# Optimization experiments

Hardware: AMD Instinct MI355X
Metric: run time of the kernel (lower is better)

## Reference

```python
import jax, jax.numpy as jnp
import numpy as np

N, E, F_IN, H, G, A, OUT = 50000, 800000, 128, 256, 64, 8, 1


def _lin(k, fi, fo):
    s = 1.0 / np.sqrt(fi)
    kw, kb = jax.random.split(k)
    W = jax.random.uniform(kw, (fi, fo), jnp.float32, -s, s)
    b = jax.random.uniform(kb, (fo,), jnp.float32, -s, s)
    return W, b


def setup_inputs() -> dict:
    key = jax.random.key(0)
    ks = jax.random.split(key, 12)
    x = jax.random.normal(ks[0], (N, F_IN), jnp.float32)
    edge_index = jax.random.randint(ks[1], (2, E), 0, N, dtype=jnp.int64)
    batch = jnp.sort(jax.random.randint(ks[2], (N,), 0, G, dtype=jnp.int64))
    graph_attr = jax.random.normal(ks[3], (G, A), jnp.float32)
    W1, b1 = _lin(ks[4], F_IN, H)
    W2, b2 = _lin(ks[5], H, H)
    W3, b3 = _lin(ks[6], H, H)
    fcW1, fcb1 = _lin(ks[7], H + A, H)
    fcW2, fcb2 = _lin(ks[8], H, OUT)
    ones = jnp.ones((H,), jnp.float32)
    zeros = jnp.zeros((H,), jnp.float32)
    return dict(x=x, graph_attr=graph_attr, edge_index=edge_index, batch=batch,
                W1=W1, b1=b1, W2=W2, b2=b2, W3=W3, b3=b3,
                g1=ones, be1=zeros, g2=ones, be2=zeros, g3=ones, be3=zeros,
                fcW1=fcW1, fcb1=fcb1, fcW2=fcW2, fcb2=fcb2)


def gcn_conv(x, W, b, src, dst, n):
    # PyG GCNConv: add self-loops, symmetric normalization, xW then scatter-add
    xw = x @ W  # [N, H]
    loop = jnp.arange(n)
    src2 = jnp.concatenate([src, loop])
    dst2 = jnp.concatenate([dst, loop])
    deg = jnp.zeros((n,), xw.dtype).at[dst2].add(1.0)
    dinv = jnp.where(deg > 0, jax.lax.rsqrt(deg), 0.0)
    norm = dinv[src2] * dinv[dst2]  # [E+N]
    out = jnp.zeros((n, xw.shape[1]), xw.dtype).at[dst2].add(xw[src2] * norm[:, None])
    return out + b


def layer_norm(x, g, b, eps=1e-5):
    m = x.mean(-1, keepdims=True)
    v = ((x - m) ** 2).mean(-1, keepdims=True)
    return (x - m) * jax.lax.rsqrt(v + eps) * g + b


def reference(x, graph_attr, edge_index, batch,
              W1, b1, W2, b2, W3, b3,
              g1, be1, g2, be2, g3, be3,
              fcW1, fcb1, fcW2, fcb2):
    src, dst = edge_index[0], edge_index[1]
    h = jax.nn.relu(layer_norm(gcn_conv(x, W1, b1, src, dst, N), g1, be1))
    h = jax.nn.relu(layer_norm(gcn_conv(h, W2, b2, src, dst, N), g2, be2))
    h = jax.nn.relu(layer_norm(gcn_conv(h, W3, b3, src, dst, N), g3, be3))
    # global mean pool over graph ids
    sums = jax.ops.segment_sum(h, batch, num_segments=G)
    cnts = jax.ops.segment_sum(jnp.ones((N,), h.dtype), batch, num_segments=G)
    pooled = sums / jnp.maximum(cnts, 1.0)[:, None]  # [G, H]
    z = jnp.concatenate([pooled, graph_attr.reshape(-1, A)], axis=1)
    z = jax.nn.relu(z @ fcW1 + fcb1)
    return z @ fcW2 + fcb2  # [G, OUT]
```

## Files before the change

### kernel.cpp

```cpp
#include <hip/hip_runtime.h>
#include <hip/hip_bf16.h>

#define N_NODES 50000
#define N_EDGES 800000
#define F_IN    128
#define H_DIM   256
#define G_NUM   64
#define A_DIM   8

#define NBUCKET 196
#define NCHUNK  391
#define CHUNK   2048
#define K4CAP   6144

typedef __attribute__((ext_vector_type(8))) short short8v;
typedef __attribute__((ext_vector_type(4))) float float4v;
typedef __attribute__((ext_vector_type(2))) float float2v;

__device__ __forceinline__ float b2f(unsigned short u) {
    return __uint_as_float(((unsigned int)u) << 16);
}
__device__ __forceinline__ unsigned short f2b(float v) {
    return __hip_bfloat16_raw(__float2bfloat16(v)).x;
}
__device__ __forceinline__ unsigned char f2fp8(float v) {
    return (unsigned char)(__builtin_amdgcn_cvt_pk_fp8_f32(v, v, 0, false) & 0xff);
}
__device__ __forceinline__ unsigned int pack2(float a, float b) {
    return (unsigned int)f2b(a) | ((unsigned int)f2b(b) << 16);
}
__device__ __forceinline__ void accadd16(float2v* a, uint4 v) {
    a[0] += __builtin_amdgcn_cvt_pk_f32_fp8((int)v.x, false);
    a[1] += __builtin_amdgcn_cvt_pk_f32_fp8((int)v.x, true);
    a[2] += __builtin_amdgcn_cvt_pk_f32_fp8((int)v.y, false);
    a[3] += __builtin_amdgcn_cvt_pk_f32_fp8((int)v.y, true);
    a[4] += __builtin_amdgcn_cvt_pk_f32_fp8((int)v.z, false);
    a[5] += __builtin_amdgcn_cvt_pk_f32_fp8((int)v.z, true);
    a[6] += __builtin_amdgcn_cvt_pk_f32_fp8((int)v.w, false);
    a[7] += __builtin_amdgcn_cvt_pk_f32_fp8((int)v.w, true);
}
__device__ __forceinline__ void accfma16(float2v* a, uint4 v, float w) {
    float2v w2 = {w, w};
    a[0] = __builtin_amdgcn_cvt_pk_f32_fp8((int)v.x, false) * w2 + a[0];
    a[1] = __builtin_amdgcn_cvt_pk_f32_fp8((int)v.x, true)  * w2 + a[1];
    a[2] = __builtin_amdgcn_cvt_pk_f32_fp8((int)v.y, false) * w2 + a[2];
    a[3] = __builtin_amdgcn_cvt_pk_f32_fp8((int)v.y, true)  * w2 + a[3];
    a[4] = __builtin_amdgcn_cvt_pk_f32_fp8((int)v.z, false) * w2 + a[4];
    a[5] = __builtin_amdgcn_cvt_pk_f32_fp8((int)v.z, true)  * w2 + a[5];
    a[6] = __builtin_amdgcn_cvt_pk_f32_fp8((int)v.w, false) * w2 + a[6];
    a[7] = __builtin_amdgcn_cvt_pk_f32_fp8((int)v.w, true)  * w2 + a[7];
}

#define SK 40


__global__ __launch_bounds__(512) void fuse0_kernel(const int* __restrict__ dst,
                                                    unsigned int* __restrict__ Hg,
                                                    const float* __restrict__ x,
                                                    const float* __restrict__ W1,
                                                    unsigned char* __restrict__ P8,
                                                    const float* __restrict__ W2,
                                                    unsigned short* __restrict__ Wt2,
                                                    const float* __restrict__ W3,
                                                    unsigned short* __restrict__ Wt3) {
    const int CB = NCHUNK;
    const int GB = (N_NODES + 127) / 128;
    int b = blockIdx.x, t = threadIdx.x;
    if (b < CB) {
        __shared__ unsigned int h[256];
        if (t < 256) h[t] = 0u;
        __syncthreads();
        int base = b * CHUNK;
        #pragma unroll
        for (int k = 0; k < 4; k++) {
            int i = base + k * 512 + t;
            if (i < N_EDGES) atomicAdd(&h[dst[i] >> 8], 1u);
        }
        __syncthreads();
        if (t < 256) Hg[(size_t)t * NCHUNK + b] = h[t];
        return;
    }
    b -= CB;
    if (b < GB) {
        __shared__ unsigned short As[128][SK];
        __shared__ unsigned short Bs[256][SK];
        int wave = t >> 6, lane = t & 63;
        int wm0 = (wave & 1) * 64, wn0 = (wave >> 1) * 64;
        int bm = b * 128;
        int l15 = lane & 15, lq = lane >> 4;
        float4v acc[4][4];
        #pragma unroll
        for (int i = 0; i < 4; i++)
            #pragma unroll
            for (int j = 0; j < 4; j++)
                acc[i][j] = (float4v){0.f, 0.f, 0.f, 0.f};

        for (int k0 = 0; k0 < F_IN; k0 += 32) {
            {
                int row = t >> 2, koff = (t & 3) * 8;
                short8v tmp = (short8v){0,0,0,0,0,0,0,0};
                if (bm + row < N_NODES) {
                    const float* xp = x + (size_t)(bm + row) * F_IN + k0 + koff;
                    float4 a0 = *(const float4*)xp;
                    float4 a1 = *(const float4*)(xp + 4);
                    tmp[0] = (short)f2b(a0.x); tmp[1] = (short)f2b(a0.y);
                    tmp[2] = (short)f2b(a0.z); tmp[3] = (short)f2b(a0.w);
                    tmp[4] = (short)f2b(a1.x); tmp[5] = (short)f2b(a1.y);
                    tmp[6] = (short)f2b(a1.z); tmp[7] = (short)f2b(a1.w);
                }
                *(short8v*)&As[row][koff] = tmp;
            }
            #pragma unroll
            for (int h = 0; h < 2; h++) {
                int c = t + h * 512;
                int n = c >> 2, koff = (c & 3) * 8;
                short8v tmp;
                #pragma unroll
                for (int kk = 0; kk < 8; kk++)
                    tmp[kk] = (short)f2b(W1[(size_t)(k0 + koff + kk) * H_DIM + n]);
                *(short8v*)&Bs[n][koff] = tmp;
            }
            __syncthreads();
            short8v af[4], bf[4];
            #pragma unroll
            for (int i = 0; i < 4; i++) {
                af[i] = *(const short8v*)&As[wm0 + i * 16 + l15][lq * 8];
                bf[i] = *(const short8v*)&Bs[wn0 + i * 16 + l15][lq * 8];
            }
            #pragma unroll
            for (int i = 0; i < 4; i++)
                #pragma unroll
                for (int j = 0; j < 4; j++)
                    acc[i][j] = __builtin_amdgcn_mfma_f32_16x16x32_bf16(af[i], bf[j], acc[i][j], 0, 0, 0);
            __syncthreads();
        }
        #pragma unroll
        for (int i = 0; i < 4; i++) {
            #pragma unroll
            for (int r = 0; r < 4; r++) {
                int row = bm + wm0 + i * 16 + lq * 4 + r;
                if (row < N_NODES) {
                    #pragma unroll
                    for (int j = 0; j < 4; j++) {
                        int col = wn0 + j * 16 + l15;
                        P8[(size_t)row * H_DIM + col] = f2fp8(acc[i][j][r]);
                    }
                }
            }
        }
        return;
    }
    b -= GB;
    int i = b * 512 + t;
    if (i < H_DIM * H_DIM) {
        int k = i >> 8, n = i & 255;
        Wt2[(size_t)n * H_DIM + k] = f2b(W2[i]);
    } else if (i < 2 * H_DIM * H_DIM) {
        int j = i - H_DIM * H_DIM;
        int k = j >> 8, n = j & 255;
        Wt3[(size_t)n * H_DIM + k] = f2b(W3[j]);
    }
}


__global__ __launch_bounds__(256) void scanH_kernel(unsigned int* __restrict__ Hg,
                                                    unsigned int* __restrict__ Btot) {
    __shared__ unsigned int tile[256];
    int b = blockIdx.x, t = threadIdx.x;
    unsigned int* row = Hg + (size_t)b * NCHUNK;
    int i0 = 2 * t, i1 = 2 * t + 1;
    unsigned int v0 = (i0 < NCHUNK) ? row[i0] : 0u;
    unsigned int v1 = (i1 < NCHUNK) ? row[i1] : 0u;
    unsigned int pair = v0 + v1;
    tile[t] = pair;
    __syncthreads();
    #pragma unroll
    for (int o = 1; o < 256; o <<= 1) {
        unsigned int add = (t >= o) ? tile[t - o] : 0u;
        __syncthreads();
        tile[t] += add;
        __syncthreads();
    }
    unsigned int excl = tile[t] - pair;
    if (i0 < NCHUNK) row[i0] = excl;
    if (i1 < NCHUNK) row[i1] = excl + v0;
    if (t == 255) Btot[b] = tile[255];
}

__global__ __launch_bounds__(256) void base_kernel(const unsigned int* __restrict__ Btot,
                                                   unsigned int* __restrict__ bucketBase,
                                                   const int* __restrict__ batch,
                                                   int* __restrict__ gstart,
                                                   int* __restrict__ rowptr,
                                                   float* __restrict__ pooled) {
    __shared__ unsigned int tile[256];
    int t = threadIdx.x;
    unsigned int v = (t < NBUCKET) ? Btot[t] : 0u;
    tile[t] = v;
    __syncthreads();
    #pragma unroll
    for (int o = 1; o < 256; o <<= 1) {
        unsigned int add = (t >= o) ? tile[t - o] : 0u;
        __syncthreads();
        tile[t] += add;
        __syncthreads();
    }
    if (t < NBUCKET) bucketBase[t] = tile[t] - v;
    if (t == NBUCKET - 1) bucketBase[NBUCKET] = tile[t];
    if (t == 0) rowptr[N_NODES] = N_EDGES;
    if (t <= G_NUM) {
        int lo = 0, hi = N_NODES;
        while (lo < hi) {
            int mid = (lo + hi) >> 1;
            if (batch[mid] < t) lo = mid + 1; else hi = mid;
        }
        gstart[t] = lo;
    }
    for (int i = t; i < G_NUM * H_DIM; i += 256) pooled[i] = 0.f;
}

__global__ __launch_bounds__(512) void scatter_kernel(const int* __restrict__ src,
                                                      const int* __restrict__ dst,
                                                      const unsigned int* __restrict__ Hg,
                                                      const unsigned int* __restrict__ bucketBase,
                                                      unsigned int* __restrict__ tmp) {
    __shared__ unsigned int off[256];
    int blk = blockIdx.x, t = threadIdx.x;
    if (t < 256)
        off[t] = (t < NBUCKET) ? (bucketBase[t] + Hg[(size_t)t * NCHUNK + blk]) : 0u;
    __syncthreads();
    int base = blk * CHUNK;
    #pragma unroll
    for (int k = 0; k < 4; k++) {
        int i = base + k * 512 + t;
        if (i < N_EDGES) {
            int d = dst[i], s = src[i];
            unsigned int slot = atomicAdd(&off[d >> 8], 1u);
            tmp[slot] = ((unsigned int)(d & 255) << 16) | (unsigned int)s;
        }
    }
}

__global__ __launch_bounds__(256) void finalize_kernel(const unsigned int* __restrict__ tmp,
                                                       const unsigned int* __restrict__ bucketBase,
                                                       int* __restrict__ rowptr,
                                                       float* __restrict__ dinv,
                                                       unsigned short* __restrict__ csr_src) {
    __shared__ unsigned int te[K4CAP];
    __shared__ unsigned int h2[256];
    __shared__ unsigned int sc[256];
    __shared__ unsigned int off2[256];
    int b = blockIdx.x, t = threadIdx.x;
    unsigned int beg = bucketBase[b], end = bucketBase[b + 1];
    int cnt = (int)(end - beg);
    bool lds_ok = (cnt <= K4CAP);
    h2[t] = 0u;
    __syncthreads();
    for (int i = t; i < cnt; i += 256) {
        unsigned int u = tmp[beg + i];
        if (lds_ok) te[i] = u;
        atomicAdd(&h2[u >> 16], 1u);
    }
    __syncthreads();
    unsigned int c = h2[t];
    sc[t] = c;
    __syncthreads();
    #pragma unroll
    for (int o = 1; o < 256; o <<= 1) {
        unsigned int add = (t >= o) ? sc[t - o] : 0u;
        __syncthreads();
        sc[t] += add;
        __syncthreads();
    }
    unsigned int excl = sc[t] - c;
    int v = (b << 8) + t;
    if (v < N_NODES) {
        rowptr[v] = (int)(beg + excl);
        dinv[v] = rsqrtf((float)c + 1.0f);
    }
    off2[t] = excl;
    __syncthreads();
    for (int i = t; i < cnt; i += 256) {
        unsigned int u = lds_ok ? te[i] : tmp[beg + i];
        unsigned int lo = u >> 16;
        unsigned int s2 = atomicAdd(&off2[lo], 1u);
        csr_src[beg + s2] = (unsigned short)(u & 0xFFFFu);
    }
}


__global__ __launch_bounds__(512) void gemm_f8(const unsigned short* __restrict__ A,
                                               const unsigned short* __restrict__ Bt,
                                               unsigned char* __restrict__ C8,
                                               const float* __restrict__ dinv,
                                               int M, int K) {
    __shared__ unsigned short As[128][SK];
    __shared__ unsigned short Bs[256][SK];
    int t = threadIdx.x;
    int wave = t >> 6, lane = t & 63;
    int wm0 = (wave & 1) * 64, wn0 = (wave >> 1) * 64;
    int bm = blockIdx.x * 128;
    int l15 = lane & 15, lq = lane >> 4;
    float4v acc[4][4];
    #pragma unroll
    for (int i = 0; i < 4; i++)
        #pragma unroll
        for (int j = 0; j < 4; j++)
            acc[i][j] = (float4v){0.f, 0.f, 0.f, 0.f};

    for (int k0 = 0; k0 < K; k0 += 32) {
        {
            int row = t >> 2, koff = (t & 3) * 8;
            uint4 va = make_uint4(0u, 0u, 0u, 0u);
            if (bm + row < M)
                va = *(const uint4*)(A + (size_t)(bm + row) * K + k0 + koff);
            *(uint4*)&As[row][koff] = va;
        }
        #pragma unroll
        for (int h = 0; h < 2; h++) {
            int c = t + h * 512;
            int row = c >> 2, koff = (c & 3) * 8;
            uint4 vb = *(const uint4*)(Bt + (size_t)row * K + k0 + koff);
            *(uint4*)&Bs[row][koff] = vb;
        }
        __syncthreads();
        short8v af[4], bf[4];
        #pragma unroll
        for (int i = 0; i < 4; i++) {
            af[i] = *(const short8v*)&As[wm0 + i * 16 + l15][lq * 8];
            bf[i] = *(const short8v*)&Bs[wn0 + i * 16 + l15][lq * 8];
        }
        #pragma unroll
        for (int i = 0; i < 4; i++)
            #pragma unroll
            for (int j = 0; j < 4; j++)
                acc[i][j] = __builtin_amdgcn_mfma_f32_16x16x32_bf16(af[i], bf[j], acc[i][j], 0, 0, 0);
        __syncthreads();
    }
    #pragma unroll
    for (int i = 0; i < 4; i++) {
        #pragma unroll
        for (int r = 0; r < 4; r++) {
            int row = bm + wm0 + i * 16 + lq * 4 + r;
            if (row < M) {
                float dv = dinv[row];
                #pragma unroll
                for (int j = 0; j < 4; j++) {
                    int col = wn0 + j * 16 + l15;
                    C8[(size_t)row * H_DIM + col] = f2fp8(dv * acc[i][j][r]);
                }
            }
        }
    }
}


template<bool W8, bool POOL>
__global__ __launch_bounds__(256) void gather_ns(const unsigned char* __restrict__ xw,
                                                 unsigned short* __restrict__ out,
                                                 const int* __restrict__ rowptr,
                                                 const unsigned short* __restrict__ csr_src,
                                                 const float* __restrict__ dinv,
                                                 const float* __restrict__ bias,
                                                 const float* __restrict__ gamma,
                                                 const float* __restrict__ beta,
                                                 const int* __restrict__ batch,
                                                 float* __restrict__ pooled) {
    __shared__ float sh[POOL ? 16 * 260 : 4];
    __shared__ int gid_s[POOL ? 16 : 4];
    int lane = threadIdx.x & 63;
    int wave = threadIdx.x >> 6;
    int p = lane & 15;
    int gbase = lane & 48;
    int nl = wave * 4 + (lane >> 4);
    int node = blockIdx.x * 16 + nl;
    int beg = rowptr[node];
    int deg = rowptr[node + 1] - beg;
    float d = dinv[node];
    const unsigned char* xp = xw + (size_t)p * 16;

    float2v acc2[8];
    #pragma unroll
    for (int k = 0; k < 8; k++) acc2[k] = (float2v){0.f, 0.f};

    {
        uint4 v = *(const uint4*)(xp + (size_t)node * H_DIM);
        if constexpr (W8) accfma16(acc2, v, d);
        else              accadd16(acc2, v);
    }

    int sv = 0; float wv = 0.f;
    if (p < deg) {
        sv = (int)csr_src[beg + p];
        if constexpr (W8) wv = dinv[sv];
    }

    for (int b0 = 0; b0 < deg; b0 += 16) {
        int m = deg - b0; if (m > 16) m = 16;
        int sv_n = 0; float wv_n = 0.f;
        int rem = deg - b0 - 16;
        if (rem > 0 && p < rem) {
            sv_n = (int)csr_src[beg + b0 + 16 + p];
            if constexpr (W8) wv_n = dinv[sv_n];
        }
        int j = 0;
        for (; j + 8 <= m; j += 8) {
            int s0 = __shfl(sv, gbase | j, 64);
            int s1 = __shfl(sv, gbase | (j + 1), 64);
            int s2 = __shfl(sv, gbase | (j + 2), 64);
            int s3 = __shfl(sv, gbase | (j + 3), 64);
            int s4 = __shfl(sv, gbase | (j + 4), 64);
            int s5 = __shfl(sv, gbase | (j + 5), 64);
            int s6 = __shfl(sv, gbase | (j + 6), 64);
            int s7 = __shfl(sv, gbase | (j + 7), 64);
            uint4 v0 = *(const uint4*)(xp + (size_t)s0 * H_DIM);
            uint4 v1 = *(const uint4*)(xp + (size_t)s1 * H_DIM);
            uint4 v2 = *(const uint4*)(xp + (size_t)s2 * H_DIM);
            uint4 v3 = *(const uint4*)(xp + (size_t)s3 * H_DIM);
            uint4 v4 = *(const uint4*)(xp + (size_t)s4 * H_DIM);
            uint4 v5 = *(const uint4*)(xp + (size_t)s5 * H_DIM);
            uint4 v6 = *(const uint4*)(xp + (size_t)s6 * H_DIM);
            uint4 v7 = *(const uint4*)(xp + (size_t)s7 * H_DIM);
            if constexpr (W8) {
                float w0 = __shfl(wv, gbase | j, 64);
                float w1 = __shfl(wv, gbase | (j + 1), 64);
                float w2 = __shfl(wv, gbase | (j + 2), 64);
                float w3 = __shfl(wv, gbase | (j + 3), 64);
                float w4 = __shfl(wv, gbase | (j + 4), 64);
                float w5 = __shfl(wv, gbase | (j + 5), 64);
                float w6 = __shfl(wv, gbase | (j + 6), 64);
                float w7 = __shfl(wv, gbase | (j + 7), 64);
                accfma16(acc2, v0, w0); accfma16(acc2, v1, w1);
                accfma16(acc2, v2, w2); accfma16(acc2, v3, w3);
                accfma16(acc2, v4, w4); accfma16(acc2, v5, w5);
                accfma16(acc2, v6, w6); accfma16(acc2, v7, w7);
            } else {
                accadd16(acc2, v0); accadd16(acc2, v1);
                accadd16(acc2, v2); accadd16(acc2, v3);
                accadd16(acc2, v4); accadd16(acc2, v5);
                accadd16(acc2, v6); accadd16(acc2, v7);
            }
        }
        for (; j + 4 <= m; j += 4) {
            int s0 = __shfl(sv, gbase | j, 64);
            int s1 = __shfl(sv, gbase | (j + 1), 64);
            int s2 = __shfl(sv, gbase | (j + 2), 64);
            int s3 = __shfl(sv, gbase | (j + 3), 64);
            uint4 v0 = *(const uint4*)(xp + (size_t)s0 * H_DIM);
            uint4 v1 = *(const uint4*)(xp + (size_t)s1 * H_DIM);
            uint4 v2 = *(const uint4*)(xp + (size_t)s2 * H_DIM);
            uint4 v3 = *(const uint4*)(xp + (size_t)s3 * H_DIM);
            if constexpr (W8) {
                float w0 = __shfl(wv, gbase | j, 64);
                float w1 = __shfl(wv, gbase | (j + 1), 64);
                float w2 = __shfl(wv, gbase | (j + 2), 64);
                float w3 = __shfl(wv, gbase | (j + 3), 64);
                accfma16(acc2, v0, w0); accfma16(acc2, v1, w1);
                accfma16(acc2, v2, w2); accfma16(acc2, v3, w3);
            } else {
                accadd16(acc2, v0); accadd16(acc2, v1);
                accadd16(acc2, v2); accadd16(acc2, v3);
            }
        }
        for (; j < m; ++j) {
            int s0 = __shfl(sv, gbase | j, 64);
            uint4 v0 = *(const uint4*)(xp + (size_t)s0 * H_DIM);
            if constexpr (W8) {
                float w0 = __shfl(wv, gbase | j, 64);
                accfma16(acc2, v0, w0);
            } else {
                accadd16(acc2, v0);
            }
        }
        sv = sv_n; wv = wv_n;
    }

    float v[16];
    #pragma unroll
    for (int k = 0; k < 8; k++) { v[2 * k] = d * acc2[k].x; v[2 * k + 1] = d * acc2[k].y; }

    #pragma unroll
    for (int q = 0; q < 4; q++) {
        float4 bi = ((const float4*)bias)[p * 4 + q];
        v[q * 4 + 0] += bi.x; v[q * 4 + 1] += bi.y;
        v[q * 4 + 2] += bi.z; v[q * 4 + 3] += bi.w;
    }
    float s = 0.f, ss = 0.f;
    #pragma unroll
    for (int k = 0; k < 16; k++) { s += v[k]; ss += v[k] * v[k]; }
    #pragma unroll
    for (int o = 1; o < 16; o <<= 1) {
        s  += __shfl_xor(s, o, 64);
        ss += __shfl_xor(ss, o, 64);
    }
    float mn = s * (1.f / H_DIM);
    float var = ss * (1.f / H_DIM) - mn * mn;
    float rstd = rsqrtf(var + 1e-5f);
    #pragma unroll
    for (int q = 0; q < 4; q++) {
        float4 ga = ((const float4*)gamma)[p * 4 + q];
        float4 be = ((const float4*)beta)[p * 4 + q];
        v[q * 4 + 0] = fmaxf((v[q * 4 + 0] - mn) * rstd * ga.x + be.x, 0.f);
        v[q * 4 + 1] = fmaxf((v[q * 4 + 1] - mn) * rstd * ga.y + be.y, 0.f);
        v[q * 4 + 2] = fmaxf((v[q * 4 + 2] - mn) * rstd * ga.z + be.z, 0.f);
        v[q * 4 + 3] = fmaxf((v[q * 4 + 3] - mn) * rstd * ga.w + be.w, 0.f);
    }

    if constexpr (POOL) {
        float* row = sh + nl * 260;
        #pragma unroll
        for (int k = 0; k < 16; k++) row[p * 16 + k] = v[k];
        if (p == 0) gid_s[nl] = batch[node];
        __syncthreads();
        int t = threadIdx.x;
        float acc = 0.f;
        int cur = gid_s[0];
        #pragma unroll
        for (int i = 0; i < 16; i++) {
            int g = gid_s[i];
            if (g != cur) {
                atomicAdd(&pooled[(size_t)cur * H_DIM + t], acc);
                acc = 0.f; cur = g;
            }
            acc += sh[i * 260 + t];
        }
        atomicAdd(&pooled[(size_t)cur * H_DIM + t], acc);
    } else {
        unsigned short* op = out + (size_t)node * H_DIM + p * 16;
        uint4 o0, o1;
        o0.x = pack2(v[0], v[1]);   o0.y = pack2(v[2], v[3]);
        o0.z = pack2(v[4], v[5]);   o0.w = pack2(v[6], v[7]);
        o1.x = pack2(v[8], v[9]);   o1.y = pack2(v[10], v[11]);
        o1.z = pack2(v[12], v[13]); o1.w = pack2(v[14], v[15]);
        *(uint4*)op = o0;
        *(uint4*)(op + 8) = o1;
    }
}


__global__ __launch_bounds__(256) void fc_kernel(const float* __restrict__ pooled,
                                                 const int* __restrict__ gstart,
                                                 const float* __restrict__ gattr,
                                                 const float* __restrict__ fcW1,
                                                 const float* __restrict__ fcb1,
                                                 const float* __restrict__ fcW2,
                                                 const float* __restrict__ fcb2,
                                                 float* __restrict__ out) {
    __shared__ float zc[H_DIM + A_DIM];
    __shared__ float z1[H_DIM];
    int g = blockIdx.x, t = threadIdx.x;
    int c_i = gstart[g + 1] - gstart[g];
    float c = (float)(c_i > 1 ? c_i : 1);
    zc[t] = pooled[(size_t)g * H_DIM + t] / c;
    if (t < A_DIM) zc[H_DIM + t] = gattr[g * A_DIM + t];
    __syncthreads();
    float s = fcb1[t];
    for (int k = 0; k < H_DIM + A_DIM; k++)
        s += zc[k] * fcW1[(size_t)k * H_DIM + t];
    z1[t] = fmaxf(s, 0.f) * fcW2[t];
    __syncthreads();
    for (int off = 128; off; off >>= 1) {
        if (t < off) z1[t] += z1[t + off];
        __syncthreads();
    }
    if (t == 0) out[g] = z1[0] + fcb2[0];
}


extern "C" void kernel_launch(void* const* d_in, const int* in_sizes, int n_in,
                              void* d_out, int out_size, void* d_ws, size_t ws_size,
                              hipStream_t stream) {
    const float* x     = (const float*)d_in[0];
    const float* gattr = (const float*)d_in[1];
    const int*   ei    = (const int*)d_in[2];
    const int*   batch = (const int*)d_in[3];
    const float* W1 = (const float*)d_in[4];  const float* b1 = (const float*)d_in[5];
    const float* W2 = (const float*)d_in[6];  const float* b2 = (const float*)d_in[7];
    const float* W3 = (const float*)d_in[8];  const float* b3 = (const float*)d_in[9];
    const float* g1 = (const float*)d_in[10]; const float* be1 = (const float*)d_in[11];
    const float* g2 = (const float*)d_in[12]; const float* be2 = (const float*)d_in[13];
    const float* g3 = (const float*)d_in[14]; const float* be3 = (const float*)d_in[15];
    const float* fcW1 = (const float*)d_in[16]; const float* fcb1 = (const float*)d_in[17];
    const float* fcW2 = (const float*)d_in[18]; const float* fcb2 = (const float*)d_in[19];
    float* out = (float*)d_out;

    char* w = (char*)d_ws;
    unsigned char*  Pb8 = (unsigned char*)w;  w += (size_t)N_NODES * H_DIM;
    unsigned short* Hb  = (unsigned short*)w; w += (size_t)N_NODES * H_DIM * 2;
    unsigned short* Wt2 = (unsigned short*)w; w += (size_t)H_DIM * H_DIM * 2;
    unsigned short* Wt3 = (unsigned short*)w; w += (size_t)H_DIM * H_DIM * 2;
    float* dinv   = (float*)w; w += (size_t)N_NODES * 4;
    float* pooled = (float*)w; w += (size_t)G_NUM * H_DIM * 4;
    int* rowptr   = (int*)w;   w += (size_t)(N_NODES + 4) * 4;
    unsigned int* Hg = (unsigned int*)w;      w += (size_t)256 * NCHUNK * 4;
    unsigned int* Btot = (unsigned int*)w;    w += (size_t)256 * 4;
    unsigned int* bucketBase = (unsigned int*)w; w += (size_t)(NBUCKET + 4) * 4;
    unsigned int* tmp = (unsigned int*)w;     w += (size_t)N_EDGES * 4;
    unsigned short* csr_src = (unsigned short*)w; w += (size_t)N_EDGES * 2;
    int* gstart   = (int*)w;   w += (size_t)(G_NUM + 1) * 4;

    const int* srcp = ei;
    const int* dstp = ei + N_EDGES;

    {
        const int CB = NCHUNK;
        const int GB = (N_NODES + 127) / 128;
        const int WB = (2 * H_DIM * H_DIM + 511) / 512;
        fuse0_kernel<<<CB + GB + WB, 512, 0, stream>>>(dstp, Hg, x, W1, Pb8, W2, Wt2, W3, Wt3);
    }
    scanH_kernel<<<NBUCKET, 256, 0, stream>>>(Hg, Btot);
    base_kernel<<<1, 256, 0, stream>>>(Btot, bucketBase, batch, gstart, rowptr, pooled);
    scatter_kernel<<<NCHUNK, 512, 0, stream>>>(srcp, dstp, Hg, bucketBase, tmp);
    finalize_kernel<<<NBUCKET, 256, 0, stream>>>(tmp, bucketBase, rowptr, dinv, csr_src);

    int gemm_blocks = (N_NODES + 127) / 128;
    int gather_blocks = N_NODES / 16;

    gather_ns<true, false><<<gather_blocks, 256, 0, stream>>>(Pb8, Hb, rowptr, csr_src,
                                                              dinv, b1, g1, be1,
                                                              nullptr, nullptr);
    gemm_f8<<<gemm_blocks, 512, 0, stream>>>(Hb, Wt2, Pb8, dinv, N_NODES, H_DIM);
    gather_ns<false, false><<<gather_blocks, 256, 0, stream>>>(Pb8, Hb, rowptr, csr_src,
                                                               dinv, b2, g2, be2,
                                                               nullptr, nullptr);
    gemm_f8<<<gemm_blocks, 512, 0, stream>>>(Hb, Wt3, Pb8, dinv, N_NODES, H_DIM);
    gather_ns<false, true><<<gather_blocks, 256, 0, stream>>>(Pb8, nullptr, rowptr, csr_src,
                                                              dinv, b3, g3, be3,
                                                              batch, pooled);
    fc_kernel<<<G_NUM, 256, 0, stream>>>(pooled, gstart, gattr, fcW1, fcb1, fcW2, fcb2, out);
}
```

Baseline: 318.2 us.

## Pipeline gather and GEMM across node quarters with double-buffered fp8 features

Splits the nodes into four quarters and launches combined kernels whose blocks gather and normalise the current quarter while other blocks run the next-layer GEMM on the previous quarter. This lets the latency-bound gather and the compute-bound GEMM overlap inside one launch. A second fp8 buffer is added so the GEMM output does not overwrite features that are still being gathered. It adds more launches, a GEMM path without LDS tiling, and some odd dead shared-memory code in the pooling gather.

```diff
diff --git a/kernel.cpp b/kernel.cpp
--- a/kernel.cpp
+++ b/kernel.cpp
@@ -12,6 +12,7 @@
 #define NCHUNK  391
 #define CHUNK   2048
 #define K4CAP   6144
+#define QN      12500
 
 typedef __attribute__((ext_vector_type(8))) short short8v;
 typedef __attribute__((ext_vector_type(4))) float float4v;
@@ -355,25 +356,69 @@
 }
 
 
-template<bool W8, bool POOL>
-__global__ __launch_bounds__(256) void gather_ns(const unsigned char* __restrict__ xw,
-                                                 unsigned short* __restrict__ out,
-                                                 const int* __restrict__ rowptr,
-                                                 const unsigned short* __restrict__ csr_src,
-                                                 const float* __restrict__ dinv,
-                                                 const float* __restrict__ bias,
-                                                 const float* __restrict__ gamma,
-                                                 const float* __restrict__ beta,
-                                                 const int* __restrict__ batch,
-                                                 float* __restrict__ pooled) {
-    __shared__ float sh[POOL ? 16 * 260 : 4];
-    __shared__ int gid_s[POOL ? 16 : 4];
-    int lane = threadIdx.x & 63;
-    int wave = threadIdx.x >> 6;
-    int p = lane & 15;
-    int gbase = lane & 48;
-    int nl = wave * 4 + (lane >> 4);
-    int node = blockIdx.x * 16 + nl;
+__device__ __forceinline__ void gemm_nl_body(const unsigned short* __restrict__ A,
+                                             const unsigned short* __restrict__ Bt,
+                                             unsigned char* __restrict__ C8,
+                                             const float* __restrict__ dinv,
+                                             int bm) {
+    int lane = threadIdx.x & 63, wave = threadIdx.x >> 6;
+    int wn0 = wave * 64;
+    int l15 = lane & 15, lq = lane >> 4;
+    float4v acc[4][4];
+    #pragma unroll
+    for (int i = 0; i < 4; i++)
+        #pragma unroll
+        for (int j = 0; j < 4; j++)
+            acc[i][j] = (float4v){0.f, 0.f, 0.f, 0.f};
+
+    const unsigned short* ar[4];
+    const unsigned short* br[4];
+    #pragma unroll
+    for (int i = 0; i < 4; i++)
+        ar[i] = A + (size_t)(bm + i * 16 + l15) * H_DIM + lq * 8;
+    #pragma unroll
+    for (int j = 0; j < 4; j++)
+        br[j] = Bt + (size_t)(wn0 + j * 16 + l15) * H_DIM + lq * 8;
+
+    for (int k0 = 0; k0 < H_DIM; k0 += 32) {
+        short8v af[4], bf[4];
+        #pragma unroll
+        for (int i = 0; i < 4; i++) af[i] = *(const short8v*)(ar[i] + k0);
+        #pragma unroll
+        for (int j = 0; j < 4; j++) bf[j] = *(const short8v*)(br[j] + k0);
+        #pragma unroll
+        for (int i = 0; i < 4; i++)
+            #pragma unroll
+            for (int j = 0; j < 4; j++)
+                acc[i][j] = __builtin_amdgcn_mfma_f32_16x16x32_bf16(af[i], bf[j], acc[i][j], 0, 0, 0);
+    }
+    #pragma unroll
+    for (int i = 0; i < 4; i++) {
+        #pragma unroll
+        for (int r = 0; r < 4; r++) {
+            int row = bm + i * 16 + lq * 4 + r;
+            if (row < N_NODES) {
+                float dv = dinv[row];
+                #pragma unroll
+                for (int j = 0; j < 4; j++) {
+                    int col = wn0 + j * 16 + l15;
+                    C8[(size_t)row * H_DIM + col] = f2fp8(dv * acc[i][j][r]);
+                }
+            }
+        }
+    }
+}
+
+
+template<bool W8>
+__device__ __forceinline__ void gather_core(const unsigned char* __restrict__ xw,
+                                            const int* __restrict__ rowptr,
+                                            const unsigned short* __restrict__ csr_src,
+                                            const float* __restrict__ dinv,
+                                            const float* __restrict__ bias,
+                                            const float* __restrict__ gamma,
+                                            const float* __restrict__ beta,
+                                            int node, int p, int gbase, float* v) {
     int beg = rowptr[node];
     int deg = rowptr[node + 1] - beg;
     float d = dinv[node];
@@ -384,9 +429,9 @@
     for (int k = 0; k < 8; k++) acc2[k] = (float2v){0.f, 0.f};
 
     {
-        uint4 v = *(const uint4*)(xp + (size_t)node * H_DIM);
-        if constexpr (W8) accfma16(acc2, v, d);
-        else              accadd16(acc2, v);
+        uint4 sv4 = *(const uint4*)(xp + (size_t)node * H_DIM);
+        if constexpr (W8) accfma16(acc2, sv4, d);
+        else              accadd16(acc2, sv4);
     }
 
     int sv = 0; float wv = 0.f;
@@ -475,7 +520,6 @@
         sv = sv_n; wv = wv_n;
     }
 
-    float v[16];
     #pragma unroll
     for (int k = 0; k < 8; k++) { v[2 * k] = d * acc2[k].x; v[2 * k + 1] = d * acc2[k].y; }
 
@@ -505,6 +549,79 @@
         v[q * 4 + 2] = fmaxf((v[q * 4 + 2] - mn) * rstd * ga.z + be.z, 0.f);
         v[q * 4 + 3] = fmaxf((v[q * 4 + 3] - mn) * rstd * ga.w + be.w, 0.f);
     }
+}
+
+__device__ __forceinline__ void store_row_bf16(unsigned short* __restrict__ out,
+                                               int node, int p, const float* v) {
+    unsigned short* op = out + (size_t)node * H_DIM + p * 16;
+    uint4 o0, o1;
+    o0.x = pack2(v[0], v[1]);   o0.y = pack2(v[2], v[3]);
+    o0.z = pack2(v[4], v[5]);   o0.w = pack2(v[6], v[7]);
+    o1.x = pack2(v[8], v[9]);   o1.y = pack2(v[10], v[11]);
+    o1.z = pack2(v[12], v[13]); o1.w = pack2(v[14], v[15]);
+    *(uint4*)op = o0;
+    *(uint4*)(op + 8) = o1;
+}
+
+
+template<bool W8>
+__global__ __launch_bounds__(256) void gg_kernel(int GBk, int nstart, int nend,
+                                                 const unsigned char* __restrict__ Pin,
+                                                 unsigned short* __restrict__ Hb,
+                                                 int mstart,
+                                                 const unsigned short* __restrict__ Wt,
+                                                 unsigned char* __restrict__ Pout,
+                                                 const int* __restrict__ rowptr,
+                                                 const unsigned short* __restrict__ csr_src,
+                                                 const float* __restrict__ dinv,
+                                                 const float* __restrict__ bias,
+                                                 const float* __restrict__ gamma,
+                                                 const float* __restrict__ beta) {
+    int b = blockIdx.x;
+    if (b < GBk) {
+        int lane = threadIdx.x & 63, wave = threadIdx.x >> 6;
+        int node = nstart + b * 16 + wave * 4 + (lane >> 4);
+        if (node >= nend) return;
+        float v[16];
+        gather_core<W8>(Pin, rowptr, csr_src, dinv, bias, gamma, beta,
+                        node, lane & 15, lane & 48, v);
+        store_row_bf16(Hb, node, lane & 15, v);
+        return;
+    }
+    gemm_nl_body(Hb, Wt, Pout, dinv, mstart + (b - GBk) * 64);
+}
+
+
+template<bool W8, bool POOL>
+__global__ __launch_bounds__(256) void gather_ns(const unsigned char* __restrict__ xw,
+                                                 unsigned short* __restrict__ out,
+                                                 const int* __restrict__ rowptr,
+                                                 const unsigned short* __restrict__ csr_src,
+                                                 const float* __restrict__ dinv,
+                                                 const float* __restrict__ bias,
+                                                 const float* __restrict__ gamma,
+                                                 const float* __restrict__ beta,
+                                                 const int* __restrict__ batch,
+                                                 float* __restrict__ pooled) {
+    __shared__ float sh[POOL ? 16 * 260 : 4];
+    __shared__ int gid_s[POOL ? 16 : 4];
+    int lane = threadIdx.x & 63;
+    int wave = threadIdx.x >> 6;
+    int p = lane & 15;
+    int nl = wave * 4 + (lane >> 4);
+    int node = blockIdx.x * 16 + nl;
+    if constexpr (POOL) {
+        for (int j = threadIdx.x; j < 2 * H_DIM; j += 256) ((float*)sh)[j * 0] = ((float*)sh)[j * 0];
+    }
+    int g0 = 0;
+    if constexpr (POOL) {
+        for (int j = threadIdx.x; j < 16 * 260; j += 256) sh[j] = 0.f;
+        g0 = batch[blockIdx.x * 16];
+        __syncthreads();
+    }
+    float v[16];
+    gather_core<W8>(xw, rowptr, csr_src, dinv, bias, gamma, beta,
+                    node, p, lane & 48, v);
 
     if constexpr (POOL) {
         float* row = sh + nl * 260;
@@ -526,14 +643,7 @@
         }
         atomicAdd(&pooled[(size_t)cur * H_DIM + t], acc);
     } else {
-        unsigned short* op = out + (size_t)node * H_DIM + p * 16;
-        uint4 o0, o1;
-        o0.x = pack2(v[0], v[1]);   o0.y = pack2(v[2], v[3]);
-        o0.z = pack2(v[4], v[5]);   o0.w = pack2(v[6], v[7]);
-        o1.x = pack2(v[8], v[9]);   o1.y = pack2(v[10], v[11]);
-        o1.z = pack2(v[12], v[13]); o1.w = pack2(v[14], v[15]);
-        *(uint4*)op = o0;
-        *(uint4*)(op + 8) = o1;
+        store_row_bf16(out, node, p, v);
     }
 }
 
@@ -585,8 +695,9 @@
     float* out = (float*)d_out;
 
     char* w = (char*)d_ws;
-    unsigned char*  Pb8 = (unsigned char*)w;  w += (size_t)N_NODES * H_DIM;
-    unsigned short* Hb  = (unsigned short*)w; w += (size_t)N_NODES * H_DIM * 2;
+    unsigned char*  Pb8  = (unsigned char*)w; w += (size_t)N_NODES * H_DIM;
+    unsigned char*  Pb8b = (unsigned char*)w; w += (size_t)N_NODES * H_DIM;
+    unsigned short* Hb   = (unsigned short*)w; w += (size_t)N_NODES * H_DIM * 2;
     unsigned short* Wt2 = (unsigned short*)w; w += (size_t)H_DIM * H_DIM * 2;
     unsigned short* Wt3 = (unsigned short*)w; w += (size_t)H_DIM * H_DIM * 2;
     float* dinv   = (float*)w; w += (size_t)N_NODES * 4;
@@ -613,19 +724,34 @@
     scatter_kernel<<<NCHUNK, 512, 0, stream>>>(srcp, dstp, Hg, bucketBase, tmp);
     finalize_kernel<<<NBUCKET, 256, 0, stream>>>(tmp, bucketBase, rowptr, dinv, csr_src);
 
-    int gemm_blocks = (N_NODES + 127) / 128;
-    int gather_blocks = N_NODES / 16;
-
-    gather_ns<true, false><<<gather_blocks, 256, 0, stream>>>(Pb8, Hb, rowptr, csr_src,
-                                                              dinv, b1, g1, be1,
-                                                              nullptr, nullptr);
-    gemm_f8<<<gemm_blocks, 512, 0, stream>>>(Hb, Wt2, Pb8, dinv, N_NODES, H_DIM);
-    gather_ns<false, false><<<gather_blocks, 256, 0, stream>>>(Pb8, Hb, rowptr, csr_src,
-                                                               dinv, b2, g2, be2,
-                                                               nullptr, nullptr);
-    gemm_f8<<<gemm_blocks, 512, 0, stream>>>(Hb, Wt3, Pb8, dinv, N_NODES, H_DIM);
-    gather_ns<false, true><<<gather_blocks, 256, 0, stream>>>(Pb8, nullptr, rowptr, csr_src,
-                                                              dinv, b3, g3, be3,
-                                                              batch, pooled);
+    const int GQB = (QN + 15) / 16;
+    const int MQB = (QN + 63) / 64;
+    const int DRB = (QN + 127) / 128;
+
+    for (int q = 0; q < 4; ++q) {
+        int MBk = (q > 0) ? MQB : 0;
+        int ns = q * QN, ms = (q - 1) * QN;
+        gg_kernel<true><<<GQB + MBk, 256, 0, stream>>>(GQB, ns, min(ns + QN, N_NODES), Pb8, Hb,
+                                                       ms, Wt2, Pb8b,
+                                                       rowptr, csr_src, dinv, b1, g1, be1);
+    }
+    gemm_f8<<<DRB, 512, 0, stream>>>(Hb + (size_t)3 * QN * H_DIM, Wt2,
+                                     Pb8b + (size_t)3 * QN * H_DIM, dinv + 3 * QN,
+                                     N_NODES - 3 * QN, H_DIM);
+
+    for (int q = 0; q < 4; ++q) {
+        int MBk = (q > 0) ? MQB : 0;
+        int ns = q * QN, ms = (q - 1) * QN;
+        gg_kernel<false><<<GQB + MBk, 256, 0, stream>>>(GQB, ns, min(ns + QN, N_NODES), Pb8b, Hb,
+                                                        ms, Wt3, Pb8,
+                                                        rowptr, csr_src, dinv, b2, g2, be2);
+    }
+    gemm_f8<<<DRB, 512, 0, stream>>>(Hb + (size_t)3 * QN * H_DIM, Wt3,
+                                     Pb8 + (size_t)3 * QN * H_DIM, dinv + 3 * QN,
+                                     N_NODES - 3 * QN, H_DIM);
+
+    gather_ns<false, true><<<N_NODES / 16, 256, 0, stream>>>(Pb8, nullptr, rowptr, csr_src,
+                                                             dinv, b3, g3, be3,
+                                                             batch, pooled);
     fc_kernel<<<G_NUM, 256, 0, stream>>>(pooled, gstart, gattr, fcW1, fcb1, fcW2, fcb2, out);
 }
```

Result: slower. 429.3 us (+34.9%).
